# Kernel optimization log

Measured on AMD Instinct MI355X. Metric: run time of the kernel, lower is better.

The kernel has to match this reference:

```python
import jax, jax.numpy as jnp
import numpy as np

G = 512      # graphs per batch
PER = 800    # nodes per graph
N = G * PER  # total nodes
X = 256      # x_size (= h_size so layers compose)
H = 256      # h_size
VOCAB = 32000
NCLS = 104


def setup_inputs() -> dict:
    rng = np.random.default_rng(0)
    # Random tree per graph: node 0 is root, parent(i) uniform in [0, i)
    i_idx = np.arange(1, PER)
    parents = np.floor(rng.random((G, PER - 1)) * i_idx).astype(np.int64)
    base = (np.arange(G) * PER)[:, None]
    edge_dst = (parents + base).reshape(-1)                     # parent (message receiver)
    edge_src = (np.tile(np.arange(1, PER), (G, 1)) + base).reshape(-1)  # child
    E = edge_src.size
    child_count = np.bincount(edge_dst, minlength=N)
    # sort edges by (dst, src) so child position = rank among siblings
    order = np.lexsort((edge_src, edge_dst))
    edge_src = edge_src[order]
    edge_dst = edge_dst[order]
    starts = np.cumsum(child_count) - child_count
    pos = np.arange(E) - starts[edge_dst]
    n = child_count[edge_dst]
    # position-dependent interpolation coefficient: n==1 -> (W_l+W_r)/2 i.e. alpha=0.5
    alpha = np.where(n == 1, 0.5, pos / np.maximum(n - 1, 1)).astype(np.float32)

    node_type = rng.integers(0, VOCAB, N).astype(np.int32)
    graph_ids = np.repeat(np.arange(G), PER).astype(np.int32)

    key = jax.random.key(0)
    ks = jax.random.split(key, 6)
    s = 0.05
    emb = jax.random.normal(ks[0], (VOCAB, X), jnp.float32) * s
    W_left = jax.random.normal(ks[1], (X, H), jnp.float32) * s
    W_right = jax.random.normal(ks[2], (X, H), jnp.float32) * s
    W_top = jax.random.normal(ks[3], (X, H), jnp.float32) * s
    b_conv = jnp.zeros((H,), jnp.float32)
    gate_w = jax.random.normal(ks[4], (H, 1), jnp.float32) * s
    gate_b = jnp.zeros((1,), jnp.float32)
    cls_w = jax.random.normal(ks[5], (H, NCLS), jnp.float32) * s
    cls_b = jnp.zeros((NCLS,), jnp.float32)

    return dict(
        node_type=jnp.asarray(node_type), edge_src=jnp.asarray(edge_src.astype(np.int32)),
        edge_dst=jnp.asarray(edge_dst.astype(np.int32)), alpha=jnp.asarray(alpha),
        child_count=jnp.asarray(child_count.astype(np.int32)), graph_ids=jnp.asarray(graph_ids),
        emb=emb, W_left=W_left, W_right=W_right, W_top=W_top, b_conv=b_conv,
        gate_w=gate_w, gate_b=gate_b, cls_w=cls_w, cls_b=cls_b,
    )


def reference(node_type, edge_src, edge_dst, alpha, child_count, graph_ids,
              emb, W_left, W_right, W_top, b_conv,
              gate_w, gate_b, cls_w, cls_b):
    h = emb[node_type]                                  # [N, X]
    # TBCNN conv layer: sum_i ((1-a_i) W_left + a_i W_right) h_child_i
    #                 = (sum (1-a_i) h_i) W_left + (sum a_i h_i) W_right
    h_src = h[edge_src]                                 # [E, X]
    left = jax.ops.segment_sum(h_src * (1.0 - alpha)[:, None], edge_dst, num_segments=N)
    right = jax.ops.segment_sum(h_src * alpha[:, None], edge_dst, num_segments=N)
    conv = jax.nn.relu(left @ W_left + right @ W_right + h @ W_top + b_conv)
    # nodes without children receive no message -> keep embedding (DGL semantics)
    h = jnp.where((child_count > 0)[:, None], conv, h)  # [N, H]

    # GlobalAttentionPooling: per-graph softmax over gate scores
    gate = h @ gate_w + gate_b                          # [N, 1]
    gmax = jax.ops.segment_max(gate, graph_ids, num_segments=G)
    e = jnp.exp(gate - gmax[graph_ids])
    denom = jax.ops.segment_sum(e, graph_ids, num_segments=G)
    attn = e / denom[graph_ids]                         # [N, 1]
    pooled = jax.ops.segment_sum(h * attn, graph_ids, num_segments=G)  # [G, H]

    return pooled @ cls_w + cls_b                       # [G, NCLS]
```

## Files before the change

### kernel.cpp

```cpp
#include <hip/hip_runtime.h>
#include <stdint.h>

#define XH   256
#define NCLS 104

typedef _Float16 half2v __attribute__((ext_vector_type(2)));
typedef _Float16 half4v __attribute__((ext_vector_type(4)));
typedef _Float16 half8v __attribute__((ext_vector_type(8)));
typedef __attribute__((ext_vector_type(4))) float floatx4;

__device__ __forceinline__ void gll16(const void* g, void* l) {
    __builtin_amdgcn_global_load_lds(
        (const __attribute__((address_space(1))) unsigned*)g,
        (__attribute__((address_space(3))) unsigned*)l, 16, 0, 0);
}
__device__ __forceinline__ float fdot2f(half2v a, half2v b, float c) {
#if __has_builtin(__builtin_amdgcn_fdot2)
    return __builtin_amdgcn_fdot2(a, b, c, false);
#else
    return c + (float)a[0] * (float)b[0] + (float)a[1] * (float)b[1];
#endif
}
__device__ __forceinline__ int MF(int x) { return (x + (x >> 2)) & 3; }


__global__ __launch_bounds__(256)
void k_prep(const float* __restrict__ Wl, const float* __restrict__ Wr,
            const float* __restrict__ Wt,
            const int* __restrict__ edge_src, const int* __restrict__ edge_dst,
            const float* __restrict__ alpha, const int* __restrict__ node_type,
            _Float16* __restrict__ Btw, int2* __restrict__ epk,
            int* __restrict__ row_start, int VQ, int E) {
    int idx = blockIdx.x * 256 + threadIdx.x;
    if (idx < 3 * XH * XH) {
        int n = idx >> 8, k = idx & 255;
        int m, c;
        if (n < 512) { m = n & 1; c = n >> 1; }
        else         { m = 2;     c = n - 512; }
        const float* W = (m == 0) ? Wl : (m == 1) ? Wr : Wt;
        Btw[idx] = (_Float16)W[k * XH + c];
        return;
    }
    idx -= 3 * XH * XH;
    if (idx < E) {
        int s  = edge_src[idx];
        float a = alpha[idx];
        int ts = node_type[s];
        int x;
        half2v w;
        if      (a == 0.0f) { x = ts * 256;          w = half2v{1.0f16, 0.0f16}; }
        else if (a == 1.0f) { x = VQ + ts * 256;     w = half2v{1.0f16, 0.0f16}; }
        else if (a == 0.5f) { x = 2 * VQ + ts * 256; w = half2v{1.0f16, 0.0f16}; }
        else { x = (ts * 256) | 1; w = half2v{(_Float16)(1.f - a), (_Float16)a}; }
        int2 p;
        p.x = x;
        p.y = __builtin_bit_cast(int, w);
        epk[idx] = p;
        int d = edge_dst[idx];
        if (idx == 0 || edge_dst[idx - 1] != d) row_start[d] = idx;
    }
}

__global__ __launch_bounds__(512, 4)
void k_main(const float* __restrict__ emb, const _Float16* __restrict__ Btw,
            const float* __restrict__ b_conv, _Float16* __restrict__ W16, int VQ) {
    __shared__ __align__(16) _Float16 Ab[32 * 256];
    __shared__ __align__(16) _Float16 Bb[768 * 32];

    const int tid  = threadIdx.x;
    const int lane = tid & 63;
    const int wv   = tid >> 6;
    const int quad = lane >> 4;
    const int l15  = lane & 15;
    const int m0   = blockIdx.x * 32;

    {
        int row = tid >> 4;
        int cg  = tid & 15;
        const float* ga = &emb[(size_t)(m0 + row) * XH + cg * 16];
        floatx4 f0 = *(const floatx4*)ga;
        floatx4 f1 = *(const floatx4*)(ga + 4);
        floatx4 f2 = *(const floatx4*)(ga + 8);
        floatx4 f3 = *(const floatx4*)(ga + 12);
        half8v h0, h1;
        #pragma unroll
        for (int i = 0; i < 4; i++) {
            h0[i] = (_Float16)f0[i]; h0[4 + i] = (_Float16)f1[i];
            h1[i] = (_Float16)f2[i]; h1[4 + i] = (_Float16)f3[i];
        }
        int g0 = cg * 2, g1 = cg * 2 + 1;
        *(half8v*)&Ab[row * 256 + (g0 >> 2) * 32 + ((g0 & 3) ^ MF(row & 15)) * 8] = h0;
        *(half8v*)&Ab[row * 256 + (g1 >> 2) * 32 + ((g1 & 3) ^ MF(row & 15)) * 8] = h1;
        _Float16* ep = &W16[(size_t)4 * VQ + (size_t)(m0 + row) * 256 + cg * 16];
        *(half8v*)ep = h0;
        *(half8v*)(ep + 8) = h1;
    }

    auto stageB = [&](int kc) {
        #pragma unroll
        for (int i = 0; i < 6; i++) {
            int grp = wv * 6 + i;
            int row = grp * 16 + (lane >> 2);
            int bd  = (lane & 3) ^ MF(row & 15);
            gll16((const char*)Btw + (size_t)row * 512 + kc * 64 + bd * 16,
                  (char*)Bb + grp * 1024);
        }
    };
    stageB(0);

    floatx4 acc[6][2];
    #pragma unroll
    for (int i = 0; i < 6; i++)
        #pragma unroll
        for (int j = 0; j < 2; j++) acc[i][j] = floatx4{0.f, 0.f, 0.f, 0.f};

    const int nbase = wv * 96;
    for (int kc = 0; kc < 8; kc++) {
        __syncthreads();
        half8v af[6], bf[2];
        #pragma unroll
        for (int nt = 0; nt < 6; nt++) {
            int row = nbase + nt * 16 + l15;
            af[nt] = *(const half8v*)&Bb[row * 32 + ((quad ^ MF(l15)) * 8)];
        }
        #pragma unroll
        for (int mt = 0; mt < 2; mt++) {
            int row = mt * 16 + l15;
            bf[mt] = *(const half8v*)&Ab[row * 256 + kc * 32 + ((quad ^ MF(l15)) * 8)];
        }
        __syncthreads();
        if (kc < 7) stageB(kc + 1);
        #pragma unroll
        for (int nt = 0; nt < 6; nt++)
            #pragma unroll
            for (int mt = 0; mt < 2; mt++)
                acc[nt][mt] = __builtin_amdgcn_mfma_f32_16x16x32_f16(af[nt], bf[mt], acc[nt][mt], 0, 0, 0);
    }

    #pragma unroll
    for (int nt = 0; nt < 6; nt++) {
        #pragma unroll
        for (int mt = 0; mt < 2; mt++) {
            int m  = mt * 16 + l15;
            int n0 = nbase + nt * 16 + quad * 4;
            half4v hv;
            #pragma unroll
            for (int r = 0; r < 4; r++) hv[r] = (_Float16)acc[nt][mt][r];
            int gs = (n0 >> 2) ^ (m & 7);
            *(half4v*)((char*)Bb + (size_t)m * 1536 + gs * 8) = hv;
        }
    }
    __syncthreads();

    #pragma unroll
    for (int it = 0; it < 4; it++) {
        int u = it * 512 + tid;
        int m = u >> 6, ns = u & 63;
        int q0 = ((ns * 8) >> 2) ^ (m & 7);
        int q1 = (((ns * 8) >> 2) + 1) ^ (m & 7);
        half4v v0 = *(const half4v*)((const char*)Bb + (size_t)m * 1536 + q0 * 8);
        half4v v1 = *(const half4v*)((const char*)Bb + (size_t)m * 1536 + q1 * 8);
        float l0 = (float)v0[0], r0 = (float)v0[1], l1 = (float)v0[2], r1 = (float)v0[3];
        float l2 = (float)v1[0], r2 = (float)v1[1], l3 = (float)v1[2], r3 = (float)v1[3];
        half4v yl = { (_Float16)l0, (_Float16)l1, (_Float16)l2, (_Float16)l3 };
        half4v yr = { (_Float16)r0, (_Float16)r1, (_Float16)r2, (_Float16)r3 };
        half4v ym = { (_Float16)(0.5f * (l0 + r0)), (_Float16)(0.5f * (l1 + r1)),
                      (_Float16)(0.5f * (l2 + r2)), (_Float16)(0.5f * (l3 + r3)) };
        size_t ro = (size_t)(m0 + m) * 256 + ns * 4;
        *(half4v*)&W16[ro]          = yl;
        *(half4v*)&W16[VQ + ro]     = yr;
        *(half4v*)&W16[2 * VQ + ro] = ym;
    }
    #pragma unroll
    for (int it = 0; it < 2; it++) {
        int u = it * 512 + tid;
        int m = u >> 5, ns = u & 31;
        int n0 = 512 + ns * 8;
        int q0 = (n0 >> 2) ^ (m & 7);
        int q1 = ((n0 >> 2) + 1) ^ (m & 7);
        half4v v0 = *(const half4v*)((const char*)Bb + (size_t)m * 1536 + q0 * 8);
        half4v v1 = *(const half4v*)((const char*)Bb + (size_t)m * 1536 + q1 * 8);
        floatx4 b0 = *(const floatx4*)&b_conv[ns * 8];
        floatx4 b1 = *(const floatx4*)&b_conv[ns * 8 + 4];
        half8v o;
        #pragma unroll
        for (int i = 0; i < 4; i++) {
            o[i]     = (_Float16)((float)v0[i] + b0[i]);
            o[4 + i] = (_Float16)((float)v1[i] + b1[i]);
        }
        *(half8v*)&W16[(size_t)3 * VQ + (size_t)(m0 + m) * 256 + ns * 8] = o;
    }
}

__global__ __launch_bounds__(1024, 8)
void k_graph(const int* __restrict__ nty, const int* __restrict__ cc,
             const _Float16* __restrict__ W16,
             const int2* __restrict__ epk, const int* __restrict__ row_start,
             const float* __restrict__ gate_w, const float* __restrict__ gate_b,
             const float* __restrict__ cls_w, const float* __restrict__ cls_b,
             float* __restrict__ out, int PER, int VQ, int E) {
    const int g    = blockIdx.x;
    const int tid  = threadIdx.x;
    const int lane = tid & 63;
    const int wv   = tid >> 6;
    const int base = g * PER;

    __shared__ float pw[16 * XH];
    __shared__ float ds[16];
    __shared__ float pooled[XH];

    float gw4[4];
    #pragma unroll
    for (int i = 0; i < 4; i++) gw4[i] = gate_w[4 * lane + i];
    const float gb = gate_b[0];

    float acc4[4] = {0.f, 0.f, 0.f, 0.f};
    float dsum = 0.f;

    int vg = base + wv;
    int c  = cc[vg];
    int tv = nty[vg];
    int rs = (c > 0) ? row_start[vg] : 0;
    half4v yt = *(const half4v*)&W16[(size_t)(c == 0 ? 4 : 3) * VQ + (size_t)tv * 256 + 4 * lane];
    int2 pd0 = epk[rs];

    for (int v = wv; v < PER; v += 16) {
        const bool has = (v + 16 < PER);
        const int vns = has ? vg + 16 : vg;
        int cn  = has ? cc[vns] : 0;
        int tvn = nty[vns];
        int rsn = (has && cn > 0) ? row_start[vns] : 0;
        half4v ytn = *(const half4v*)&W16[(size_t)(cn == 0 ? 4 : 3) * VQ + (size_t)tvn * 256 + 4 * lane];
        int2 pdn = epk[rsn];

        float h4[4];
        if (c == 0) {
            #pragma unroll
            for (int i = 0; i < 4; i++) h4[i] = (float)yt[i];
        } else {
            float s4[4] = {0.f, 0.f, 0.f, 0.f};
            int e = rs;
            const int e1 = rs + c;
            int2 p0 = pd0;
            while (e + 2 <= e1) {
                int2 p1 = epk[e + 1];
                int2 pn = epk[min(e + 2, E - 1)];
                int off0 = p0.x & ~1, d0 = (p0.x & 1) ? VQ : 0;
                int off1 = p1.x & ~1, d1 = (p1.x & 1) ? VQ : 0;
                half4v a0 = *(const half4v*)&W16[(size_t)off0 + 4 * lane];
                half4v b0 = *(const half4v*)&W16[(size_t)(off0 + d0) + 4 * lane];
                half4v a1 = *(const half4v*)&W16[(size_t)off1 + 4 * lane];
                half4v b1 = *(const half4v*)&W16[(size_t)(off1 + d1) + 4 * lane];
                half2v w0 = __builtin_bit_cast(half2v, p0.y);
                half2v w1 = __builtin_bit_cast(half2v, p1.y);
                #pragma unroll
                for (int i = 0; i < 4; i++)
                    s4[i] = fdot2f(half2v{a0[i], b0[i]}, w0, s4[i]);
                #pragma unroll
                for (int i = 0; i < 4; i++)
                    s4[i] = fdot2f(half2v{a1[i], b1[i]}, w1, s4[i]);
                p0 = pn;
                e += 2;
            }
            if (e < e1) {
                int off0 = p0.x & ~1, d0 = (p0.x & 1) ? VQ : 0;
                half4v a0 = *(const half4v*)&W16[(size_t)off0 + 4 * lane];
                half4v b0 = *(const half4v*)&W16[(size_t)(off0 + d0) + 4 * lane];
                half2v w0 = __builtin_bit_cast(half2v, p0.y);
                #pragma unroll
                for (int i = 0; i < 4; i++)
                    s4[i] = fdot2f(half2v{a0[i], b0[i]}, w0, s4[i]);
            }
            #pragma unroll
            for (int i = 0; i < 4; i++)
                h4[i] = fmaxf(s4[i] + (float)yt[i], 0.f);
        }

        float sg = h4[0] * gw4[0] + h4[1] * gw4[1] + h4[2] * gw4[2] + h4[3] * gw4[3];
        #pragma unroll
        for (int o = 1; o < 64; o <<= 1) sg += __shfl_xor(sg, o);
        float ew = __expf(sg + gb);
        dsum += ew;
        #pragma unroll
        for (int i = 0; i < 4; i++) acc4[i] += ew * h4[i];

        c = cn; rs = rsn; yt = ytn; pd0 = pdn; vg = vns;
    }

    #pragma unroll
    for (int i = 0; i < 4; i++) pw[wv * XH + 4 * lane + i] = acc4[i];
    if (lane == 0) ds[wv] = dsum;
    __syncthreads();

    if (tid < XH) {
        float p = 0.f, d = 0.f;
        #pragma unroll
        for (int w = 0; w < 16; w++) p += pw[w * XH + tid];
        #pragma unroll
        for (int w = 0; w < 16; w++) d += ds[w];
        pooled[tid] = p / d;
    }
    __syncthreads();

    if (tid < NCLS) {
        float o = cls_b[tid];
        #pragma unroll 8
        for (int k = 0; k < XH; k++) o += pooled[k] * cls_w[k * NCLS + tid];
        out[g * NCLS + tid] = o;
    }
}

extern "C" void kernel_launch(void* const* d_in, const int* in_sizes, int n_in,
                              void* d_out, int out_size, void* d_ws, size_t ws_size,
                              hipStream_t stream) {
    const int*   node_type   = (const int*)d_in[0];
    const int*   edge_src    = (const int*)d_in[1];
    const int*   edge_dst    = (const int*)d_in[2];
    const float* alpha       = (const float*)d_in[3];
    const int*   child_count = (const int*)d_in[4];
    const float* emb         = (const float*)d_in[6];
    const float* Wl          = (const float*)d_in[7];
    const float* Wr          = (const float*)d_in[8];
    const float* Wt          = (const float*)d_in[9];
    const float* b_conv      = (const float*)d_in[10];
    const float* gate_w      = (const float*)d_in[11];
    const float* gate_b      = (const float*)d_in[12];
    const float* cls_w       = (const float*)d_in[13];
    const float* cls_b       = (const float*)d_in[14];

    const int N     = in_sizes[0];
    const int E     = in_sizes[1];
    const int vocab = in_sizes[6] / XH;
    const int G     = out_size / NCLS;
    const int PER   = N / G;
    const int VQ    = vocab * 256;

    _Float16* W16 = (_Float16*)d_ws;
    _Float16* Btw = W16 + (size_t)5 * VQ;
    int2*     epk = (int2*)(Btw + 3 * XH * XH);
    int*      row_start = (int*)(epk + E);

    hipLaunchKernelGGL(k_prep, dim3((3 * XH * XH + E + 255) / 256), dim3(256), 0, stream,
                       Wl, Wr, Wt, edge_src, edge_dst, alpha, node_type,
                       Btw, epk, row_start, VQ, E);

    hipLaunchKernelGGL(k_main, dim3(vocab / 32), dim3(512), 0, stream,
                       emb, Btw, b_conv, W16, VQ);

    hipLaunchKernelGGL(k_graph, dim3(G), dim3(1024), 0, stream,
                       node_type, child_count, W16, epk, row_start,
                       gate_w, gate_b, cls_w, cls_b, (float*)d_out, PER, VQ, E);
}
```

Baseline: 234.8 us.

## Process two nodes per wavefront with half-wave lanes and 16-byte loads

Each 64-lane wavefront is split into two 32-lane halves, and each half handles its own node. Every lane now owns 8 of the 256 features through half8v loads, so there are 32 node slots per block instead of 16. The child loop becomes a wave-uniform __any loop with predication, and the edge-pair prefetch now loads the first two edges of the next node. The type/bias row is no longer prefetched one iteration ahead. The aim is more memory-level parallelism and wider gathers in the latency-bound gather loop. The cost is divergence when the two half-waves have different child counts, a larger shared-memory reduction, and more registers.

```diff
diff --git a/kernel.cpp b/kernel.cpp
--- a/kernel.cpp
+++ b/kernel.cpp
@@ -198,106 +198,110 @@
              const int2* __restrict__ epk, const int* __restrict__ row_start,
              const float* __restrict__ gate_w, const float* __restrict__ gate_b,
              const float* __restrict__ cls_w, const float* __restrict__ cls_b,
-             float* __restrict__ out, int PER, int VQ, int E) {
+             float* __restrict__ out, int PER, int VQ) {
     const int g    = blockIdx.x;
     const int tid  = threadIdx.x;
     const int lane = tid & 63;
-    const int wv   = tid >> 6;
+    const int l32  = lane & 31;
+    const int slot = (tid >> 6) * 2 + (lane >> 5);
     const int base = g * PER;
 
-    __shared__ float pw[16 * XH];
-    __shared__ float ds[16];
+    __shared__ float pw[32 * XH];
+    __shared__ float ds[32];
     __shared__ float pooled[XH];
 
-    float gw4[4];
-    #pragma unroll
-    for (int i = 0; i < 4; i++) gw4[i] = gate_w[4 * lane + i];
+    float gw8[8];
+    #pragma unroll
+    for (int i = 0; i < 8; i++) gw8[i] = gate_w[8 * l32 + i];
     const float gb = gate_b[0];
 
-    float acc4[4] = {0.f, 0.f, 0.f, 0.f};
+    float acc8[8] = {0.f, 0.f, 0.f, 0.f, 0.f, 0.f, 0.f, 0.f};
     float dsum = 0.f;
 
-    int vg = base + wv;
+    int vg = base + slot;
     int c  = cc[vg];
     int tv = nty[vg];
     int rs = (c > 0) ? row_start[vg] : 0;
-    half4v yt = *(const half4v*)&W16[(size_t)(c == 0 ? 4 : 3) * VQ + (size_t)tv * 256 + 4 * lane];
     int2 pd0 = epk[rs];
-
-    for (int v = wv; v < PER; v += 16) {
-        const bool has = (v + 16 < PER);
-        const int vns = has ? vg + 16 : vg;
+    int2 pd1 = epk[rs + (c > 1 ? 1 : 0)];
+
+    for (int v = slot; v < PER; v += 32) {
+        const bool has = (v + 32 < PER);
+        const int vns = has ? vg + 32 : vg;
         int cn  = has ? cc[vns] : 0;
         int tvn = nty[vns];
         int rsn = (has && cn > 0) ? row_start[vns] : 0;
-        half4v ytn = *(const half4v*)&W16[(size_t)(cn == 0 ? 4 : 3) * VQ + (size_t)tvn * 256 + 4 * lane];
-        int2 pdn = epk[rsn];
-
-        float h4[4];
+        int2 pdn0 = epk[rsn];
+        int2 pdn1 = epk[rsn + (cn > 1 ? 1 : 0)];
+
+        half8v yt = *(const half8v*)&W16[(size_t)(c == 0 ? 4 : 3) * VQ + (size_t)tv * 256 + 8 * l32];
+
+        float s8[8] = {0.f, 0.f, 0.f, 0.f, 0.f, 0.f, 0.f, 0.f};
+        int e = rs;
+        const int e1 = rs + c;
+        int2 p0 = pd0, p1 = pd1;
+        while (__any(e < e1)) {
+            if (e < e1) {
+                int2 np0 = epk[min(e + 2, e1 - 1)];
+                int2 np1 = epk[min(e + 3, e1 - 1)];
+                int off0 = p0.x & ~1, d0 = (p0.x & 1) ? VQ : 0;
+                half8v a0 = *(const half8v*)&W16[(size_t)off0 + 8 * l32];
+                half8v b0 = *(const half8v*)&W16[(size_t)(off0 + d0) + 8 * l32];
+                half2v w0 = __builtin_bit_cast(half2v, p0.y);
+                if (e + 1 < e1) {
+                    int off1 = p1.x & ~1, d1 = (p1.x & 1) ? VQ : 0;
+                    half8v a1 = *(const half8v*)&W16[(size_t)off1 + 8 * l32];
+                    half8v b1 = *(const half8v*)&W16[(size_t)(off1 + d1) + 8 * l32];
+                    half2v w1 = __builtin_bit_cast(half2v, p1.y);
+                    #pragma unroll
+                    for (int i = 0; i < 8; i++)
+                        s8[i] = fdot2f(half2v{a0[i], b0[i]}, w0, s8[i]);
+                    #pragma unroll
+                    for (int i = 0; i < 8; i++)
+                        s8[i] = fdot2f(half2v{a1[i], b1[i]}, w1, s8[i]);
+                } else {
+                    #pragma unroll
+                    for (int i = 0; i < 8; i++)
+                        s8[i] = fdot2f(half2v{a0[i], b0[i]}, w0, s8[i]);
+                }
+                p0 = np0; p1 = np1;
+                e += 2;
+            }
+        }
+
+        float h8[8];
         if (c == 0) {
             #pragma unroll
-            for (int i = 0; i < 4; i++) h4[i] = (float)yt[i];
+            for (int i = 0; i < 8; i++) h8[i] = (float)yt[i];
         } else {
-            float s4[4] = {0.f, 0.f, 0.f, 0.f};
-            int e = rs;
-            const int e1 = rs + c;
-            int2 p0 = pd0;
-            while (e + 2 <= e1) {
-                int2 p1 = epk[e + 1];
-                int2 pn = epk[min(e + 2, E - 1)];
-                int off0 = p0.x & ~1, d0 = (p0.x & 1) ? VQ : 0;
-                int off1 = p1.x & ~1, d1 = (p1.x & 1) ? VQ : 0;
-                half4v a0 = *(const half4v*)&W16[(size_t)off0 + 4 * lane];
-                half4v b0 = *(const half4v*)&W16[(size_t)(off0 + d0) + 4 * lane];
-                half4v a1 = *(const half4v*)&W16[(size_t)off1 + 4 * lane];
-                half4v b1 = *(const half4v*)&W16[(size_t)(off1 + d1) + 4 * lane];
-                half2v w0 = __builtin_bit_cast(half2v, p0.y);
-                half2v w1 = __builtin_bit_cast(half2v, p1.y);
-                #pragma unroll
-                for (int i = 0; i < 4; i++)
-                    s4[i] = fdot2f(half2v{a0[i], b0[i]}, w0, s4[i]);
-                #pragma unroll
-                for (int i = 0; i < 4; i++)
-                    s4[i] = fdot2f(half2v{a1[i], b1[i]}, w1, s4[i]);
-                p0 = pn;
-                e += 2;
-            }
-            if (e < e1) {
-                int off0 = p0.x & ~1, d0 = (p0.x & 1) ? VQ : 0;
-                half4v a0 = *(const half4v*)&W16[(size_t)off0 + 4 * lane];
-                half4v b0 = *(const half4v*)&W16[(size_t)(off0 + d0) + 4 * lane];
-                half2v w0 = __builtin_bit_cast(half2v, p0.y);
-                #pragma unroll
-                for (int i = 0; i < 4; i++)
-                    s4[i] = fdot2f(half2v{a0[i], b0[i]}, w0, s4[i]);
-            }
             #pragma unroll
-            for (int i = 0; i < 4; i++)
-                h4[i] = fmaxf(s4[i] + (float)yt[i], 0.f);
-        }
-
-        float sg = h4[0] * gw4[0] + h4[1] * gw4[1] + h4[2] * gw4[2] + h4[3] * gw4[3];
-        #pragma unroll
-        for (int o = 1; o < 64; o <<= 1) sg += __shfl_xor(sg, o);
+            for (int i = 0; i < 8; i++) h8[i] = fmaxf(s8[i] + (float)yt[i], 0.f);
+        }
+
+        float sg = 0.f;
+        #pragma unroll
+        for (int i = 0; i < 8; i++) sg += h8[i] * gw8[i];
+        #pragma unroll
+        for (int o = 1; o < 32; o <<= 1) sg += __shfl_xor(sg, o);
         float ew = __expf(sg + gb);
         dsum += ew;
         #pragma unroll
-        for (int i = 0; i < 4; i++) acc4[i] += ew * h4[i];
-
-        c = cn; rs = rsn; yt = ytn; pd0 = pdn; vg = vns;
-    }
-
-    #pragma unroll
-    for (int i = 0; i < 4; i++) pw[wv * XH + 4 * lane + i] = acc4[i];
-    if (lane == 0) ds[wv] = dsum;
+        for (int i = 0; i < 8; i++) acc8[i] += ew * h8[i];
+
+        c = cn; tv = tvn; rs = rsn; pd0 = pdn0; pd1 = pdn1; vg = vns;
+    }
+
+    #pragma unroll
+    for (int i = 0; i < 8; i++) pw[slot * XH + 8 * l32 + i] = acc8[i];
+    if (l32 == 0) ds[slot] = dsum;
     __syncthreads();
 
     if (tid < XH) {
         float p = 0.f, d = 0.f;
         #pragma unroll
-        for (int w = 0; w < 16; w++) p += pw[w * XH + tid];
-        #pragma unroll
-        for (int w = 0; w < 16; w++) d += ds[w];
+        for (int w = 0; w < 32; w++) p += pw[w * XH + tid];
+        #pragma unroll
+        for (int w = 0; w < 32; w++) d += ds[w];
         pooled[tid] = p / d;
     }
     __syncthreads();
@@ -349,5 +353,5 @@
 
     hipLaunchKernelGGL(k_graph, dim3(G), dim3(1024), 0, stream,
                        node_type, child_count, W16, epk, row_start,
-                       gate_w, gate_b, cls_w, cls_b, (float*)d_out, PER, VQ, E);
-}
+                       gate_w, gate_b, cls_w, cls_b, (float*)d_out, PER, VQ);
+}
```

After: 387.1 us. 64.9% more time.
